# Optimization experiments

Measured on AMD Instinct MI355X. Metric: run time of the kernel, lower is better.

## Reference

```python
import jax, jax.numpy as jnp
import numpy as np

WS = 128          # crop window size
EPS = 1e-06


def setup_inputs() -> dict:
    key = jax.random.key(0)
    ks = jax.random.split(key, 8)
    E, S, K, H, W, HID = 32, 2, 256, 384, 384, 128
    x = jax.random.normal(ks[0], (E, H, W), jnp.float32)
    sigma = jax.random.uniform(ks[1], (S, H, W), jnp.float32)
    c = jax.random.normal(ks[2], (K, E), jnp.float32)
    centroids = jax.random.randint(ks[3], (K, 2), 0, H).astype(jnp.int32)
    M = jax.random.uniform(ks[4], (K, K), jnp.float32)  # sigmoid affinities in [0,1]
    din = E + S
    W1 = jax.random.normal(ks[5], (din, HID), jnp.float32) / np.sqrt(din)
    W2 = jax.random.normal(ks[6], (HID, HID), jnp.float32) / np.sqrt(HID)
    W3 = jax.random.normal(ks[7], (HID, 1), jnp.float32) / np.sqrt(HID)
    return {"x": x, "sigma": sigma, "c": c, "centroids": centroids, "M": M,
            "W1": W1, "b1": jnp.zeros((HID,), jnp.float32),
            "W2": W2, "b2": jnp.zeros((HID,), jnp.float32),
            "W3": W3, "b3": jnp.zeros((1,), jnp.float32)}


def reference(x, sigma, c, M, W1, b1, W2, b2, W3, b3, centroids):
    E, h, w = x.shape
    K = c.shape[0]
    ws, half = WS, WS // 2

    # ---- centre_crop: per-seed clamped top-left + mesh-grid indices ----
    cy = jnp.clip(centroids[:, 0], half, h - half)           # [K]
    cx = jnp.clip(centroids[:, 1], half, w - half)
    ty, tx = cy - half, cx - half                             # top-left (y, x)
    ar = jnp.arange(ws, dtype=jnp.int32)
    gy = jnp.broadcast_to(ty[:, None, None] + ar[None, :, None], (K, ws, ws))
    gx = jnp.broadcast_to(tx[:, None, None] + ar[None, None, :], (K, ws, ws))

    # ---- feature_engineering: gather crops, subtract seed embedding ----
    feats = jnp.concatenate([x, sigma], axis=0)               # [E+S, h, w]
    crops = feats[:, gy, gx]                                  # [E+S, K, ws, ws]
    crops = jnp.moveaxis(crops, 0, 1)                         # [K, E+S, ws, ws]
    crops = crops.at[:, :E].add(-c[:, :, None, None])

    # ---- pixel_classifier: per-pixel MLP -> logit ----
    pix = jnp.moveaxis(crops, 1, -1)                          # [K, ws, ws, E+S]
    h1 = jax.nn.relu(pix @ W1 + b1)
    h2 = jax.nn.relu(h1 @ W2 + b2)
    dist = (h2 @ W3 + b3)[..., 0]                             # [K, ws, ws]

    # ---- _gate_by_center_logit: logit(sig(a)*sig(b)) = a+b-softplus(logaddexp(a,b)) ----
    cyi = (centroids[:, 0] - ty).astype(jnp.int32)
    cxi = (centroids[:, 1] - tx).astype(jnp.int32)
    center = dist[jnp.arange(K), cyi, cxi]                    # [K]
    b = center[:, None, None]
    dist = dist + b - jax.nn.softplus(jnp.logaddexp(dist, b))

    # ---- apply_seed_merging: scatter to [K, h*w], affinity-weighted merge, gather ----
    Ms = 0.5 * (M + M.T)
    Ms = Ms.at[jnp.diag_indices(K)].set(1.0)
    pix_idx = (gy * w + gx).reshape(K, ws * ws)               # unique within each crop
    rows = jnp.arange(K)[:, None]
    logits = jnp.zeros((K, h * w), dist.dtype).at[rows, pix_idx].set(dist.reshape(K, -1))
    has = jnp.zeros((K, h * w), dist.dtype).at[rows, pix_idx].set(1.0)
    merged = (Ms @ logits) / jnp.clip(Ms @ has, EPS, None)
    out = merged[rows, pix_idx].reshape(K, 1, ws, ws)
    return out
```

## Files before the change

kernel.cpp:

```cpp
#include <hip/hip_runtime.h>
#include <hip/hip_bf16.h>


#define HH    384
#define WW    384
#define NE    32
#define NK    256
#define HALF  64
#define HWSZ  (HH * WW)
#define EPSV  1e-6f
#define CAPX  192

typedef _Float16 half8 __attribute__((ext_vector_type(8)));
typedef _Float16 half2v __attribute__((ext_vector_type(2)));
typedef float floatx4 __attribute__((ext_vector_type(4)));

#define MFMA16(a, b, c) __builtin_amdgcn_mfma_f32_16x16x32_f16((a), (b), (c), 0, 0, 0)

__device__ __forceinline__ half2v pk_f16(float a, float b) {
    return __builtin_bit_cast(half2v, __builtin_amdgcn_cvt_pkrtz(a, b));
}

__device__ __forceinline__ int row_order(int ri) {
    return (ri & 1) ? (191 - (ri >> 1)) : (192 + (ri >> 1));
}

#define WS_DIST   0
#define WS_MSYM   4194304
#define WS_W2F    4259840
#define WS_D      4268032
#define WS_CENTER 4284416
#define WS_G      5026560

__global__ void prepg_kernel(const float* __restrict__ M, const float* __restrict__ W1,
                             const float* __restrict__ W2, const float* __restrict__ c,
                             const float* __restrict__ b1,
                             const float* __restrict__ x, const float* __restrict__ sigma,
                             float* __restrict__ Msym, _Float16* __restrict__ W2f,
                             _Float16* __restrict__ D, _Float16* __restrict__ G) {
    const int bid = blockIdx.x;
    const int tid = threadIdx.x;
    if (bid < 256) {
        int idx = bid * 256 + tid;
        {
            int i = idx >> 8, j = idx & 255;
            Msym[idx] = (i == j) ? 1.0f : 0.5f * (M[i * NK + j] + M[j * NK + i]);
        }
        if (idx < 2048) {
            int l = idx & 63;
            int col = ((idx >> 8) << 4) + (l & 15);
            int kb = ((idx >> 6) & 3) * 32 + 8 * (l >> 4);
            #pragma unroll
            for (int j = 0; j < 8; ++j)
                W2f[idx * 8 + j] = (_Float16)W2[(kb + j) * 128 + col];
        }
        if (idx < 32768) {
            int k = idx >> 7, h = idx & 127;
            float s = -b1[h];
            #pragma unroll 8
            for (int e = 0; e < NE; ++e) s = fmaf(c[k * NE + e], W1[e * 128 + h], s);
            D[idx] = (_Float16)s;
        }
    } else {
        int px = (bid - 256) * 256 + tid;
        float f[34];
        #pragma unroll
        for (int e = 0; e < NE; ++e) f[e] = x[e * HWSZ + px];
        f[32] = sigma[px];
        f[33] = sigma[HWSZ + px];
        _Float16* gp = G + (size_t)px * 128;
        #pragma unroll 1
        for (int h0 = 0; h0 < 128; h0 += 8) {
            half8 hv;
            #pragma unroll
            for (int j = 0; j < 8; ++j) {
                float z = 0.0f;
                const float* w1 = W1 + (h0 + j);
                #pragma unroll
                for (int e = 0; e < 34; ++e) z = fmaf(f[e], w1[e * 128], z);
                hv[j] = (_Float16)z;
            }
            *(half8*)(gp + h0) = hv;
        }
    }
}

__global__ __launch_bounds__(128)
void center2_kernel(const _Float16* __restrict__ G, const _Float16* __restrict__ D,
                    const float* __restrict__ W2, const float* __restrict__ b2,
                    const float* __restrict__ W3, const float* __restrict__ b3,
                    const int* __restrict__ cent, float* __restrict__ center) {
    __shared__ float h1s[128];
    __shared__ float red[2];
    int k = blockIdx.x, j = threadIdx.x;
    int cy0 = cent[2 * k], cx0 = cent[2 * k + 1];
    const _Float16* g = G + ((size_t)cy0 * WW + cx0) * 128;
    h1s[j] = fmaxf((float)g[j] - (float)D[k * 128 + j], 0.0f);
    __syncthreads();
    float acc = 0.0f;
    #pragma unroll 8
    for (int i = 0; i < 128; ++i) acc = fmaf(h1s[i], W2[i * 128 + j], acc);
    float p = fmaxf(acc + b2[j], 0.0f) * W3[j];
    #pragma unroll
    for (int m = 1; m < 64; m <<= 1) p += __shfl_xor(p, m, 64);
    if ((j & 63) == 0) red[j >> 6] = p;
    __syncthreads();
    if (j == 0) center[k] = red[0] + red[1] + b3[0];
}

__global__ __launch_bounds__(64)
void pix_kernel(const _Float16* __restrict__ G, const _Float16* __restrict__ D,
                const _Float16* __restrict__ W2f, const int* __restrict__ cent,
                const float* __restrict__ b2, const float* __restrict__ W3,
                float* __restrict__ dist) {
    __shared__ int sjw[CAPX];

    const int l   = threadIdx.x;
    const int lg  = l >> 4;
    const int xi  = l & 15;

    const int bid = blockIdx.x;
    const int r   = row_order(bid / 24);
    const int wx0 = (bid % 24) * 16;

    int nc;
    {
        int base = 0;
        const int2* c2 = (const int2*)cent;
        #pragma unroll
        for (int cch = 0; cch < 4; ++cch) {
            int j = cch * 64 + l;
            int2 cc = c2[j];
            int ty = min(max(cc.x, HALF), HH - HALF) - HALF;
            int tx = min(max(cc.y, HALF), WW - HALF) - HALF;
            bool f = (r >= ty) && (r < ty + 128) &&
                     (tx <= wx0 + 15) && (tx + 127 >= wx0);
            unsigned long long m = __ballot(f);
            int pos = base + __popcll(m & ((1ull << l) - 1ull));
            if (f && pos < CAPX) sjw[pos] = (j << 20) | (ty << 10) | tx;
            base += __popcll(m);
        }
        nc = min(base, CAPX);
    }

    half8 B2w[8][4];
    const half8* W2f8 = (const half8*)W2f;
    #pragma unroll
    for (int n = 0; n < 8; ++n)
        #pragma unroll
        for (int s = 0; s < 4; ++s) B2w[n][s] = W2f8[(n * 4 + s) * 64 + l];

    float b2v[8][4];
    half2v w3pk[8][2];
    #pragma unroll
    for (int n = 0; n < 8; ++n) {
        #pragma unroll
        for (int q = 0; q < 4; ++q) b2v[n][q] = b2[16 * n + 4 * lg + q];
        #pragma unroll
        for (int q = 0; q < 2; ++q)
            w3pk[n][q] = half2v{(_Float16)W3[16 * n + 4 * lg + 2 * q],
                                (_Float16)W3[16 * n + 4 * lg + 2 * q + 1]};
    }

    half8 gA[4];
    {
        const char* Gb = (const char*)G + ((size_t)r * WW + wx0 + xi) * 256 + lg * 16;
        #pragma unroll
        for (int s = 0; s < 4; ++s) gA[s] = *(const half8*)(Gb + s * 64);
    }
    const half8 hz = half8{};

    #pragma unroll 1
    for (int i = 0; i < nc; ++i) {
        int cp = sjw[i];
        int tx = cp & 1023, ty = (cp >> 10) & 1023, j = cp >> 20;

        const char* Dp = (const char*)D + j * 256 + lg * 16;
        half8 hin[4];
        #pragma unroll
        for (int s = 0; s < 4; ++s) {
            half8 dv = *(const half8*)(Dp + s * 64);
            hin[s] = __builtin_elementwise_max(gA[s] - dv, hz);
        }

        float p = 0.0f;
        __builtin_amdgcn_s_setprio(1);
        #pragma unroll
        for (int n = 0; n < 8; ++n) {
            floatx4 acc = floatx4{b2v[n][0], b2v[n][1], b2v[n][2], b2v[n][3]};
            #pragma unroll
            for (int s = 0; s < 4; ++s)
                acc = MFMA16(B2w[n][s], hin[s], acc);
            half2v h0 = __builtin_elementwise_max(pk_f16(acc[0], acc[1]), half2v{});
            half2v h1 = __builtin_elementwise_max(pk_f16(acc[2], acc[3]), half2v{});
            p = __builtin_amdgcn_fdot2(h0, w3pk[n][0], p, false);
            p = __builtin_amdgcn_fdot2(h1, w3pk[n][1], p, false);
        }
        __builtin_amdgcn_s_setprio(0);
        p += __shfl_xor(p, 16, 64);
        p += __shfl_xor(p, 32, 64);

        if (lg == 0) {
            int xcol = wx0 + xi;
            unsigned dx = (unsigned)(xcol - tx);
            if (dx < 128u)
                dist[((size_t)j << 14) + ((r - ty) << 7) + (int)dx] = p;
        }
    }
}

__global__ __launch_bounds__(256)
void merge_kernel(const float* __restrict__ dist, const int* __restrict__ cent,
                  const float* __restrict__ Msym, const float* __restrict__ center,
                  const float* __restrict__ b3, float* __restrict__ out) {
    __shared__ _Float16 dl[CAPX][64];
    __shared__ int   sjw[CAPX];
    __shared__ short stx[CAPX];
    __shared__ float smv[4][2][CAPX];
    __shared__ int   scnt;

    const int tid = threadIdx.x;
    const int l   = tid & 63;
    const int wv  = tid >> 6;
    const int r   = row_order(blockIdx.x / 6);
    const int xt  = blockIdx.x % 6;
    const int px  = xt * 64 + l;
    const float b3s = b3[0];

    if (wv == 0) {
        int base = 0;
        const int2* c2 = (const int2*)cent;
        #pragma unroll
        for (int cch = 0; cch < 4; ++cch) {
            int j = cch * 64 + l;
            int2 cc = c2[j];
            int ty = min(max(cc.x, HALF), HH - HALF) - HALF;
            int tx = min(max(cc.y, HALF), WW - HALF) - HALF;
            bool f = (r >= ty) && (r < ty + 128) &&
                     (tx <= xt * 64 + 63) && (tx + 127 >= xt * 64);
            unsigned long long m = __ballot(f);
            int pos = base + __popcll(m & ((1ull << l) - 1ull));
            if (f && pos < CAPX) sjw[pos] = (j << 20) | (ty << 10) | tx;
            base += __popcll(m);
        }
        if (l == 0) scnt = min(base, CAPX);
    }
    __syncthreads();
    const int nc = scnt;

    #pragma unroll 1
    for (int j = wv; j < nc; j += 4) {
        int cp = sjw[j];
        int tx = cp & 1023, ty = (cp >> 10) & 1023, jj = cp >> 20;
        stx[j] = (short)tx;
        unsigned dx = (unsigned)(px - tx);
        float v = 0.0f;
        if (dx < 128u) {
            float d = dist[((size_t)jj << 14) + ((r - ty) << 7) + (int)dx] + b3s;
            float bc = center[jj];
            float mm = fmaxf(fmaxf(d, bc), 0.0f);
            float lgv = mm + __logf(__expf(0.0f - mm) + __expf(d - mm) +
                                    __expf(bc - mm));
            v = d + bc - lgv;
        }
        dl[j][l] = (_Float16)v;
    }
    __syncthreads();

    auto gatherM = [&](int t, float* mv) {
        if (t < nc) {
            const float* mrow = Msym + (sjw[t] >> 20) * NK;
            #pragma unroll
            for (int cch = 0; cch < 3; ++cch) {
                int j2 = cch * 64 + l;
                mv[cch] = (j2 < nc) ? mrow[sjw[j2] >> 20] : 0.0f;
            }
        }
    };

    float mv[3];
    gatherM(wv, mv);
    int cur = 0;
    #pragma unroll 1
    for (int t = wv; t < nc; t += 4) {
        #pragma unroll
        for (int cch = 0; cch < 3; ++cch) {
            int j2 = cch * 64 + l;
            if (j2 < CAPX) smv[wv][cur][j2] = mv[cch];
        }
        gatherM(t + 4, mv);

        int cpt = sjw[t];
        float num = 0.0f, den = 0.0f;
        #pragma unroll 4
        for (int j = 0; j < nc; ++j) {
            float m = smv[wv][cur][j];
            num = fmaf(m, (float)dl[j][l], num);
            unsigned dxj = (unsigned)(px - (int)stx[j]);
            den += (dxj < 128u) ? m : 0.0f;
        }
        unsigned dxk = (unsigned)(px - (cpt & 1023));
        if (dxk < 128u)
            out[((size_t)(cpt >> 20) << 14) + ((r - ((cpt >> 10) & 1023)) << 7) + (int)dxk] =
                num / fmaxf(den, EPSV);
        cur ^= 1;
    }
}

extern "C" void kernel_launch(void* const* d_in, const int* in_sizes, int n_in,
                              void* d_out, int out_size, void* d_ws, size_t ws_size,
                              hipStream_t stream) {
    const float* x     = (const float*)d_in[0];
    const float* sigma = (const float*)d_in[1];
    const float* c     = (const float*)d_in[2];
    const int*   cent  = (const int*)d_in[3];
    const float* M     = (const float*)d_in[4];
    const float* W1    = (const float*)d_in[5];
    const float* b1    = (const float*)d_in[6];
    const float* W2    = (const float*)d_in[7];
    const float* b2    = (const float*)d_in[8];
    const float* W3    = (const float*)d_in[9];
    const float* b3    = (const float*)d_in[10];
    float* out = (float*)d_out;

    float* ws       = (float*)d_ws;
    float* dist     = ws + WS_DIST;
    float* Msym     = ws + WS_MSYM;
    _Float16* W2f   = (_Float16*)(ws + WS_W2F);
    _Float16* D     = (_Float16*)(ws + WS_D);
    float* center   = ws + WS_CENTER;
    _Float16* G     = (_Float16*)(ws + WS_G);

    prepg_kernel<<<832, 256, 0, stream>>>(M, W1, W2, c, b1, x, sigma,
                                          Msym, W2f, D, G);
    center2_kernel<<<256, 128, 0, stream>>>(G, D, W2, b2, W3, b3, cent, center);
    pix_kernel<<<9216, 64, 0, stream>>>(G, D, W2f, cent, b2, W3, dist);
    merge_kernel<<<2304, 256, 0, stream>>>(dist, cent, Msym, center, b3, out);
}
```

Measured before the change: 274.5 us.

## Compute seed-merge numerator and denominator with fp16 MFMA tiles

```diff
diff --git a/kernel.cpp b/kernel.cpp
--- a/kernel.cpp
+++ b/kernel.cpp
@@ -10,6 +10,7 @@
 #define HWSZ  (HH * WW)
 #define EPSV  1e-6f
 #define CAPX  192
+#define NCP   200
 
 typedef _Float16 half8 __attribute__((ext_vector_type(8)));
 typedef _Float16 half2v __attribute__((ext_vector_type(2)));
@@ -213,18 +214,18 @@
 void merge_kernel(const float* __restrict__ dist, const int* __restrict__ cent,
                   const float* __restrict__ Msym, const float* __restrict__ center,
                   const float* __restrict__ b3, float* __restrict__ out) {
-    __shared__ _Float16 dl[CAPX][64];
+    __shared__ _Float16 XTl[128][NCP];
+    __shared__ _Float16 mmt[2][16][NCP];
     __shared__ int   sjw[CAPX];
-    __shared__ short stx[CAPX];
-    __shared__ float smv[4][2][CAPX];
     __shared__ int   scnt;
 
     const int tid = threadIdx.x;
     const int l   = tid & 63;
     const int wv  = tid >> 6;
+    const int lg  = l >> 4;
+    const int xi  = l & 15;
     const int r   = row_order(blockIdx.x / 6);
     const int xt  = blockIdx.x % 6;
-    const int px  = xt * 64 + l;
     const float b3s = b3[0];
 
     if (wv == 0) {
@@ -246,15 +247,17 @@
         if (l == 0) scnt = min(base, CAPX);
     }
     __syncthreads();
-    const int nc = scnt;
+    const int nc  = scnt;
+    if (nc == 0) return;
+    const int ncw = (nc + 31) & ~31;
+    const int px  = xt * 64 + l;
 
     #pragma unroll 1
     for (int j = wv; j < nc; j += 4) {
         int cp = sjw[j];
         int tx = cp & 1023, ty = (cp >> 10) & 1023, jj = cp >> 20;
-        stx[j] = (short)tx;
         unsigned dx = (unsigned)(px - tx);
-        float v = 0.0f;
+        float v = 0.0f, hv = 0.0f;
         if (dx < 128u) {
             float d = dist[((size_t)jj << 14) + ((r - ty) << 7) + (int)dx] + b3s;
             float bc = center[jj];
@@ -262,48 +265,66 @@
             float lgv = mm + __logf(__expf(0.0f - mm) + __expf(d - mm) +
                                     __expf(bc - mm));
             v = d + bc - lgv;
-        }
-        dl[j][l] = (_Float16)v;
-    }
+            hv = 1.0f;
+        }
+        XTl[l][j]      = (_Float16)v;
+        XTl[64 + l][j] = (_Float16)hv;
+    }
+    #pragma unroll 1
+    for (int j = nc + wv; j < ncw; j += 4) {
+        XTl[l][j]      = (_Float16)0.0f;
+        XTl[64 + l][j] = (_Float16)0.0f;
+    }
+
+    const int ntt = (nc + 15) >> 4;
+    const int ks  = ncw >> 5;
+
+    auto gatherM = [&](int tt, int buf) {
+        if (tt >= ntt) return;
+        int tl = tid >> 4;
+        int tg = tt * 16 + tl;
+        int kt = (tg < nc) ? (sjw[tg] >> 20) : -1;
+        const float* mrow = Msym + kt * NK;
+        for (int j = tid & 15; j < ncw; j += 16) {
+            float mv = 0.0f;
+            if (kt >= 0 && j < nc) mv = mrow[sjw[j] >> 20];
+            mmt[buf][tl][j] = (_Float16)mv;
+        }
+    };
+
+    gatherM(0, 0);
     __syncthreads();
 
-    auto gatherM = [&](int t, float* mv) {
-        if (t < nc) {
-            const float* mrow = Msym + (sjw[t] >> 20) * NK;
-            #pragma unroll
-            for (int cch = 0; cch < 3; ++cch) {
-                int j2 = cch * 64 + l;
-                mv[cch] = (j2 < nc) ? mrow[sjw[j2] >> 20] : 0.0f;
+    #pragma unroll 1
+    for (int tt = 0; tt < ntt; ++tt) {
+        int buf = tt & 1;
+        gatherM(tt + 1, buf ^ 1);
+
+        floatx4 accN = floatx4{0.0f, 0.0f, 0.0f, 0.0f};
+        floatx4 accD = accN;
+        #pragma unroll 1
+        for (int s = 0; s < ks; ++s) {
+            half8 a  = *(const half8*)&mmt[buf][xi][32 * s + 8 * lg];
+            half8 bN = *(const half8*)&XTl[16 * wv + xi][32 * s + 8 * lg];
+            half8 bD = *(const half8*)&XTl[64 + 16 * wv + xi][32 * s + 8 * lg];
+            accN = MFMA16(a, bN, accN);
+            accD = MFMA16(a, bD, accD);
+        }
+
+        #pragma unroll
+        for (int q = 0; q < 4; ++q) {
+            int tg = tt * 16 + 4 * lg + q;
+            if (tg < nc) {
+                int cp = sjw[tg];
+                int tx = cp & 1023, ty = (cp >> 10) & 1023, kt = cp >> 20;
+                int gp = xt * 64 + 16 * wv + xi;
+                unsigned dx = (unsigned)(gp - tx);
+                if (dx < 128u)
+                    out[((size_t)kt << 14) + ((r - ty) << 7) + (int)dx] =
+                        accN[q] / fmaxf(accD[q], EPSV);
             }
         }
-    };
-
-    float mv[3];
-    gatherM(wv, mv);
-    int cur = 0;
-    #pragma unroll 1
-    for (int t = wv; t < nc; t += 4) {
-        #pragma unroll
-        for (int cch = 0; cch < 3; ++cch) {
-            int j2 = cch * 64 + l;
-            if (j2 < CAPX) smv[wv][cur][j2] = mv[cch];
-        }
-        gatherM(t + 4, mv);
-
-        int cpt = sjw[t];
-        float num = 0.0f, den = 0.0f;
-        #pragma unroll 4
-        for (int j = 0; j < nc; ++j) {
-            float m = smv[wv][cur][j];
-            num = fmaf(m, (float)dl[j][l], num);
-            unsigned dxj = (unsigned)(px - (int)stx[j]);
-            den += (dxj < 128u) ? m : 0.0f;
-        }
-        unsigned dxk = (unsigned)(px - (cpt & 1023));
-        if (dxk < 128u)
-            out[((size_t)(cpt >> 20) << 14) + ((r - ((cpt >> 10) & 1023)) << 7) + (int)dxk] =
-                num / fmaxf(den, EPSV);
-        cur ^= 1;
+        __syncthreads();
     }
 }
 
```

Result: faster. 267.4 us (-2.6%).
